# Performance work log

Measured on AMD Instinct MI355X. Metric: run time of the kernel, lower is better.

The kernel has to match this reference:

```python
import jax, jax.numpy as jnp
import numpy as np

D, K, CIN, CD, COUT = 3, 16, 128, 32, 256
C = CIN + CD                  # 160 = C_in + C_delta after concat
DM = -(-COUT // C)            # depth_multiplier = ceil(C_out / C) = 2
N, I = 4, 2048                # batch, points per cloud; M = N*I = 8192


def _bn(x, g, b, eps=1e-5):
    # BatchNorm1d in training mode: biased batch statistics over dim 0
    mu = x.mean(0)
    v = x.var(0)
    return (x - mu) * jax.lax.rsqrt(v + eps) * g + b


def _knn(p, k):
    # knn_graph over ALL M points (wrapper passes no batch vector), loop=True
    d2 = jnp.sum(p * p, axis=1)
    dist = d2[:, None] + d2[None, :] - 2.0 * (p @ p.T)   # [M,M]
    _, idx = jax.lax.top_k(-dist, k)                     # [M,K], self first
    return idx


def _gconv(t, w, b, M):
    # grouped Conv1d(K, K*K, kernel=K, groups=K): t [M,K,K], w [K(cin), K(out/grp), K(tap)]
    return jnp.einsum('mcl,col->mco', t, w).reshape(M, K * K) + b


def _xconv(xf, pf, idx, w1a, b1a, g1a, be1a, w1b, b1b, g1b, be1b,
           w2, b2, g2a, be2a, wc2a, bc2a, g2b, be2b, wc2b, bc2b, g2c, be2c,
           wcd, bcd, wl, bl):
    M = pf.shape[0]
    rel = pf[idx] - pf[:, None, :]                       # [M,K,D] relative neighbor coords
    # mlp1: lift relative coords to C_delta features
    h = rel.reshape(M * K, D)
    h = _bn(jax.nn.elu(h @ w1a + b1a), g1a, be1a)
    h = _bn(jax.nn.elu(h @ w1b + b1b), g1b, be1b)
    x_star = jnp.concatenate([h.reshape(M, K, CD), xf[idx]], axis=-1)  # [M,K,C]
    x_star = x_star.transpose(0, 2, 1)                   # [M,C,K]
    # mlp2: learn KxK X-transformation from the K*D relative coords
    t = _bn(jax.nn.elu(rel.reshape(M, K * D) @ w2 + b2), g2a, be2a).reshape(M, K, K)
    t = _bn(jax.nn.elu(_gconv(t, wc2a, bc2a, M)), g2b, be2b).reshape(M, K, K)
    t = _bn(_gconv(t, wc2b, bc2b, M), g2c, be2c).reshape(M, K, K)
    xt = jnp.einsum('mck,mkj->mcj', x_star, t)           # [M,C,K] batched matmul
    # depthwise Conv1d(C, C*DM, K, groups=C) collapses K, then final Linear
    y = jnp.einsum('mcl,col->mco', xt, wcd).reshape(M, C * DM) + bcd
    return y @ wl + bl                                   # [M,COUT]


def setup_inputs() -> dict:
    key = jax.random.key(0)
    ks = jax.random.split(key, 16)
    r = lambda k, s: jax.random.normal(k, s, jnp.float32) * 0.1
    return dict(
        x=jax.random.normal(ks[0], (N, I, CIN), jnp.float32),
        pos=jax.random.normal(ks[1], (N, I, D), jnp.float32),
        w1a=r(ks[2], (D, CD)), b1a=r(ks[3], (CD,)), g1a=jnp.ones((CD,)), be1a=jnp.zeros((CD,)),
        w1b=r(ks[4], (CD, CD)), b1b=r(ks[5], (CD,)), g1b=jnp.ones((CD,)), be1b=jnp.zeros((CD,)),
        w2=r(ks[6], (D * K, K * K)), b2=r(ks[7], (K * K,)), g2a=jnp.ones((K * K,)), be2a=jnp.zeros((K * K,)),
        wc2a=r(ks[8], (K, K, K)), bc2a=r(ks[9], (K * K,)), g2b=jnp.ones((K * K,)), be2b=jnp.zeros((K * K,)),
        wc2b=r(ks[10], (K, K, K)), bc2b=r(ks[11], (K * K,)), g2c=jnp.ones((K * K,)), be2c=jnp.zeros((K * K,)),
        wcd=r(ks[12], (C, DM, K)), bcd=r(ks[13], (C * DM,)),
        wl=r(ks[14], (C * DM, COUT)), bl=r(ks[15], (COUT,)),
    )


def reference(x, pos, w1a, b1a, g1a, be1a, w1b, b1b, g1b, be1b,
              w2, b2, g2a, be2a, wc2a, bc2a, g2b, be2b, wc2b, bc2b, g2c, be2c,
              wcd, bcd, wl, bl):
    pf = pos.reshape(N * I, D)
    xf = x.reshape(N * I, CIN)
    idx = _knn(pf, K)
    out = _xconv(xf, pf, idx, w1a, b1a, g1a, be1a, w1b, b1b, g1b, be1b,
                 w2, b2, g2a, be2a, wc2a, bc2a, g2b, be2b, wc2b, bc2b, g2c, be2c,
                 wcd, bcd, wl, bl)
    return out.reshape(N, I, COUT)
```

## Files before the change

### kernel.cpp

```cpp
#include <hip/hip_runtime.h>
#include <math.h>

#define M_PTS 8192
#define MK    131072

typedef __attribute__((ext_vector_type(8))) short bf16x8;
typedef __attribute__((ext_vector_type(4))) float f32x4;
typedef __fp16 half2v __attribute__((ext_vector_type(2)));
union H2U { half2v h; unsigned u; };

__device__ __forceinline__ float elu(float v){ return v > 0.f ? v : __expf(v)-1.0f; }

__device__ __forceinline__ unsigned cvt_pk_bf16(float lo, float hi){
  unsigned r;
  asm("v_cvt_pk_bf16_f32 %0, %1, %2" : "=v"(r) : "v"(lo), "v"(hi));
  return r;
}
__device__ __forceinline__ unsigned pk_min_u16(unsigned a, unsigned b){
  unsigned r; asm("v_pk_min_u16 %0, %1, %2" : "=v"(r) : "v"(a), "v"(b)); return r;
}
__device__ __forceinline__ unsigned pk_max_u16(unsigned a, unsigned b){
  unsigned r; asm("v_pk_max_u16 %0, %1, %2" : "=v"(r) : "v"(a), "v"(b)); return r;
}

__device__ __forceinline__ unsigned distkey(float4 c, float qx, float qy, float qz, float d2q){
  #pragma clang fp contract(off)
  float dot  = __builtin_fmaf(c.z, qz, __builtin_fmaf(c.y, qy, __builtin_fmaf(c.x, qx, 0.0f)));
  float A    = d2q + c.w;
  float B    = 2.0f * dot;
  float dist = A - B;
  unsigned u = __float_as_uint(dist);
  return u ^ ((unsigned)((int)u >> 31) | 0x80000000u);
}

__global__ __launch_bounds__(256) void knn_kernel(const float* __restrict__ pos,
                                                  int* __restrict__ nidx,
                                                  float* __restrict__ st){
  __shared__ float4 cand[1024];
  __shared__ unsigned long long hits[4][64];
  int tid  = threadIdx.x;
  int lane = tid & 63;
  int wv   = tid >> 6;
  int q    = blockIdx.x*4 + wv;
  if (blockIdx.x == 0){
    for (int i = tid; i < 2048; i += 256) st[i] = 0.f;
  }
  float qx = pos[3*q], qy = pos[3*q+1], qz = pos[3*q+2];
  float d2q;
  {
    #pragma clang fp contract(off)
    d2q = (qx*qx + qy*qy) + qz*qz;
  }

  unsigned ka[8];
  #pragma unroll
  for (int s=0;s<8;s++) ka[s] = 0xFFFFFFFFu;

  for (int base = 0; base < M_PTS; base += 1024){
    for (int t = tid; t < 1024; t += 256){
      #pragma clang fp contract(off)
      int j = base + t;
      float x = pos[3*j], y = pos[3*j+1], z = pos[3*j+2];
      float d2v = (x*x + y*y) + z*z;
      cand[t] = make_float4(x,y,z,d2v);
    }
    __syncthreads();
    #pragma unroll
    for (int k=0; k<8; k++){
      float4 c0 = cand[lane + k*128];
      float4 c1 = cand[lane + 64 + k*128];
      float dotA = c0.x*qx + c0.y*qy + c0.z*qz;
      float dotB = c1.x*qx + c1.y*qy + c1.z*qz;
      float dA = fmaxf((d2q + c0.w) - 2.0f*dotA, 0.f);
      float dB = fmaxf((d2q + c1.w) - 2.0f*dotB, 0.f);
      H2U pu; pu.h = __builtin_amdgcn_cvt_pkrtz(dA, dB);
      unsigned v = pu.u;
      #pragma unroll
      for (int s=0;s<8;s++){
        unsigned mn = pk_min_u16(v, ka[s]);
        unsigned mx = pk_max_u16(v, ka[s]);
        ka[s] = mn; v = mx;
      }
    }
    __syncthreads();
  }

  unsigned lo[8], hi[8];
  #pragma unroll
  for (int s=0;s<8;s++){ lo[s] = ka[s] & 0xFFFFu; hi[s] = ka[s] >> 16; }
  unsigned t16 = 0xFFFFu;
  for (int r=0; r<16; r++){
    unsigned head = min(lo[0], hi[0]);
    unsigned best = head;
    #pragma unroll
    for (int off=32; off>0; off>>=1){
      unsigned o = __shfl_xor(best, off, 64);
      best = min(best, o);
    }
    bool adv = (head == best);
    bool fromLo = lo[0] <= hi[0];
    bool aL = adv && fromLo;
    bool aH = adv && !fromLo;
    #pragma unroll
    for (int s=0;s<7;s++){
      lo[s] = aL ? lo[s+1] : lo[s];
      hi[s] = aH ? hi[s+1] : hi[s];
    }
    lo[7] = aL ? 0xFFFFu : lo[7];
    hi[7] = aH ? 0xFFFFu : hi[7];
    t16 = best;
  }
  unsigned tu = min(t16 + 2u, 0x7C00u);
  float thrF;
  asm("v_cvt_f32_f16 %0, %1" : "=v"(thrF) : "v"(tu));

  int cnt = 0;
  for (int base = 0; base < M_PTS; base += 1024){
    for (int t = tid; t < 1024; t += 256){
      #pragma clang fp contract(off)
      int j = base + t;
      float x = pos[3*j], y = pos[3*j+1], z = pos[3*j+2];
      float d2v = (x*x + y*y) + z*z;
      cand[t] = make_float4(x,y,z,d2v);
    }
    __syncthreads();
    #pragma unroll
    for (int k=0; k<16; k++){
      int idx = lane + k*64;
      int j = base + idx;
      float4 c = cand[idx];
      float dot = c.x*qx + c.y*qy + c.z*qz;
      bool hit = ((d2q + c.w) - 2.0f*dot) <= thrF;
      unsigned long long m = __ballot(hit);
      if (m){
        unsigned u = distkey(c, qx, qy, qz, d2q);
        if (hit){
          int slot = cnt + __popcll(m & ((1ull<<lane)-1ull));
          if (slot < 64) hits[wv][slot] = ((unsigned long long)u << 32) | (unsigned)j;
        }
        cnt += (int)__popcll(m);
      }
    }
    __syncthreads();
  }

  int cc = min(cnt, 64);
  unsigned long long mine = (lane < cc) ? hits[wv][lane] : ~0ull;
  for (int r=0; r<16; r++){
    unsigned long long best = mine;
    #pragma unroll
    for (int off=32; off>0; off>>=1){
      unsigned long long o = __shfl_xor(best, off, 64);
      best = (o < best) ? o : best;
    }
    if (mine == best) mine = ~0ull;
    if (lane == 0) nidx[q*16 + r] = (int)(unsigned)best;
  }
}

#define COMPUTE_RELF_8()                                              \
  for (int f = tid; f < 8*48; f += 256){                              \
    int p = f/48, kd = f%48, k = kd/3, d = kd%3;                      \
    int j = nidx[(m0+p)*16 + k];                                      \
    relf[p][kd] = pos[3*j+d] - pos[3*(m0+p)+d];                       \
  }                                                                   \
  __syncthreads();

#define COMPUTE_T1_8(acc)                                             \
  _Pragma("unroll")                                                   \
  for (int p=0;p<8;p++) acc[p] = b2[tid];                             \
  for (int kk=0; kk<48; kk++){                                        \
    float w = w2[kk*256 + tid];                                       \
    _Pragma("unroll")                                                 \
    for (int p=0;p<8;p++) acc[p] += relf[p][kk]*w;                    \
  }

__global__ __launch_bounds__(256) void stats_a_kernel(const float* __restrict__ pos,
    const int* __restrict__ nidx,
    const float* __restrict__ w1a, const float* __restrict__ b1a,
    const float* __restrict__ w2,  const float* __restrict__ b2,
    const float* __restrict__ wl,  unsigned short* __restrict__ wlbf,
    float* __restrict__ tact,
    float* __restrict__ s1, float* __restrict__ s3){
  int tid = threadIdx.x;
  if (blockIdx.x < 512){
    __shared__ float relS[256][3];
    __shared__ float red[8][64];
    int r = blockIdx.x*256 + tid;
    int m = r >> 4;
    int j = nidx[r];
    relS[tid][0] = pos[3*j  ]-pos[3*m  ];
    relS[tid][1] = pos[3*j+1]-pos[3*m+1];
    relS[tid][2] = pos[3*j+2]-pos[3*m+2];
    __syncthreads();
    int c = tid & 31, g = tid >> 5;
    float w0=w1a[c], w1v=w1a[32+c], w2v=w1a[64+c], b=b1a[c];
    float s=0.f, q=0.f;
    for (int rr=g*32; rr<g*32+32; rr++){
      float h = elu(b + relS[rr][0]*w0 + relS[rr][1]*w1v + relS[rr][2]*w2v);
      s += h; q += h*h;
    }
    red[g][c]=s; red[g][32+c]=q;
    __syncthreads();
    if (tid < 64){
      float a=0.f;
      #pragma unroll
      for (int gg=0;gg<8;gg++) a += red[gg][tid];
      atomicAdd(&s1[tid], a);
    }
  } else if (blockIdx.x < 1536){
    __shared__ float relf[8][48];
    int m0 = (blockIdx.x-512)*8;
    COMPUTE_RELF_8();
    float acc[8];
    COMPUTE_T1_8(acc);
    float s=0.f, q=0.f;
    #pragma unroll
    for (int p=0;p<8;p++){
      float v = elu(acc[p]);
      s += v; q += v*v;
      tact[(size_t)(m0+p)*256 + tid] = v;
    }
    atomicAdd(&s3[tid], s); atomicAdd(&s3[256+tid], q);
  } else {
    int t = (blockIdx.x - 1536)*256 + tid;
    int lane = t & 63;
    int fr   = t >> 6;
    int k0   = (fr >> 4)*32 + (lane >> 4)*8;
    int col  = (fr & 15)*16 + (lane & 15);
    const float* wp = wl + (size_t)k0*256 + col;
    uint4 v;
    v.x = cvt_pk_bf16(wp[0],    wp[256]);
    v.y = cvt_pk_bf16(wp[512],  wp[768]);
    v.z = cvt_pk_bf16(wp[1024], wp[1280]);
    v.w = cvt_pk_bf16(wp[1536], wp[1792]);
    ((uint4*)wlbf)[t] = v;
  }
}

__global__ __launch_bounds__(256) void stats_b_kernel(const float* __restrict__ pos,
    const int* __restrict__ nidx,
    const float* __restrict__ w1a, const float* __restrict__ b1a,
    const float* __restrict__ s1,  const float* __restrict__ g1a, const float* __restrict__ be1a,
    const float* __restrict__ w1b, const float* __restrict__ b1b,
    float* __restrict__ tact,
    const float* __restrict__ s3,  const float* __restrict__ g2a, const float* __restrict__ be2a,
    const float* __restrict__ wc2a,const float* __restrict__ bc2a,
    float* __restrict__ s2, float* __restrict__ s4){
  int tid = threadIdx.x;
  const float invMK = 1.f/(float)MK;
  const float invM  = 1.f/8192.f;
  if (blockIdx.x < 2048){
    __shared__ float xnS[64][33];
    __shared__ float red[8][64];
    __shared__ float muA[32], ivA[32];
    if (tid < 32){
      float mu  = s1[tid]*invMK;
      float var = s1[32+tid]*invMK - mu*mu;
      muA[tid] = mu; ivA[tid] = rsqrtf(var+1e-5f)*g1a[tid];
    }
    __syncthreads();
    {
      int rl = tid >> 2;
      int r  = blockIdx.x*64 + rl;
      int m = r >> 4;
      int j = nidx[r];
      float rx = pos[3*j]-pos[3*m], ry = pos[3*j+1]-pos[3*m+1], rz = pos[3*j+2]-pos[3*m+2];
      int c0 = (tid & 3)*8;
      #pragma unroll
      for (int u=0; u<8; u++){
        int cc = c0 + u;
        float h = elu(b1a[cc] + rx*w1a[cc] + ry*w1a[32+cc] + rz*w1a[64+cc]);
        xnS[rl][cc] = (h-muA[cc])*ivA[cc] + be1a[cc];
      }
    }
    __syncthreads();
    int o = tid & 31, g = tid >> 5;
    float wcol[32];
    #pragma unroll
    for (int cc=0;cc<32;cc++) wcol[cc] = w1b[cc*32+o];
    float bo = b1b[o], s=0.f, q=0.f;
    for (int rr=g*8; rr<g*8+8; rr++){
      float a = bo;
      #pragma unroll
      for (int cc=0;cc<32;cc++) a += xnS[rr][cc]*wcol[cc];
      float v = elu(a);
      s += v; q += v*v;
    }
    red[g][o]=s; red[g][32+o]=q;
    __syncthreads();
    if (tid < 64){
      float a=0.f;
      #pragma unroll
      for (int gg=0;gg<8;gg++) a += red[gg][tid];
      atomicAdd(&s2[tid], a);
    }
  } else {
    __shared__ float tn[8][256];
    int m0 = (blockIdx.x-2048)*8;
    float mu3  = s3[tid]*invM;
    float var3 = s3[256+tid]*invM - mu3*mu3;
    float i3   = rsqrtf(var3+1e-5f)*g2a[tid];
    float bb3  = be2a[tid];
    float tv[8];
    #pragma unroll
    for (int p=0;p<8;p++) tv[p] = tact[(size_t)(m0+p)*256 + tid];
    #pragma unroll
    for (int p=0;p<8;p++) tn[p][tid] = (tv[p]-mu3)*i3 + bb3;
    __syncthreads();
    int c = tid >> 4;
    float wreg[16];
    const float4* wv4 = (const float4*)(wc2a + tid*16);
    #pragma unroll
    for (int v=0; v<4; v++){ float4 f = wv4[v]; wreg[4*v]=f.x; wreg[4*v+1]=f.y; wreg[4*v+2]=f.z; wreg[4*v+3]=f.w; }
    float bias = bc2a[tid];
    float s=0.f, q=0.f;
    #pragma unroll
    for (int p=0;p<8;p++){
      float a2 = bias;
      #pragma unroll
      for (int l=0;l<16;l++) a2 += tn[p][c*16+l]*wreg[l];
      float v = elu(a2);
      s += v; q += v*v;
      tv[p] = v;
    }
    #pragma unroll
    for (int p=0;p<8;p++) tact[(size_t)(m0+p)*256 + tid] = tv[p];
    atomicAdd(&s4[tid], s); atomicAdd(&s4[256+tid], q);
  }
}

__global__ __launch_bounds__(256) void t3_stats_kernel(
    float* __restrict__ tact,
    const float* __restrict__ s4, const float* __restrict__ g2b, const float* __restrict__ be2b,
    const float* __restrict__ wc2b, const float* __restrict__ bc2b, float* __restrict__ s5){
  __shared__ float tn2[8][256];
  int m0 = blockIdx.x*8, tid = threadIdx.x;
  const float invM = 1.f/8192.f;
  float mu4  = s4[tid]*invM;
  float var4 = s4[256+tid]*invM - mu4*mu4;
  float i4   = rsqrtf(var4+1e-5f)*g2b[tid];
  float bb4  = be2b[tid];
  float tv[8];
  #pragma unroll
  for (int p=0;p<8;p++) tv[p] = tact[(size_t)(m0+p)*256 + tid];
  #pragma unroll
  for (int p=0;p<8;p++) tn2[p][tid] = (tv[p]-mu4)*i4 + bb4;
  __syncthreads();
  int c = tid >> 4;
  float w2reg[16];
  { const float4* wv4 = (const float4*)(wc2b + tid*16);
    #pragma unroll
    for (int v=0; v<4; v++){ float4 f = wv4[v]; w2reg[4*v]=f.x; w2reg[4*v+1]=f.y; w2reg[4*v+2]=f.z; w2reg[4*v+3]=f.w; } }
  float bias2 = bc2b[tid];
  float s=0.f, q=0.f;
  #pragma unroll
  for (int p=0;p<8;p++){
    float a3 = bias2;
    #pragma unroll
    for (int l=0;l<16;l++) a3 += tn2[p][c*16+l]*w2reg[l];
    s += a3; q += a3*a3;
    tv[p] = a3;
  }
  #pragma unroll
  for (int p=0;p<8;p++) tact[(size_t)(m0+p)*256 + tid] = tv[p];
  atomicAdd(&s5[tid], s); atomicAdd(&s5[256+tid], q);
}

#define PF8 8
__global__ __launch_bounds__(256) void final_mfma_kernel(
    const float* __restrict__ x, const float* __restrict__ pos, const int* __restrict__ nidx,
    const float* __restrict__ w1a, const float* __restrict__ b1a,
    const float* __restrict__ g1a, const float* __restrict__ be1a,
    const float* __restrict__ w1b, const float* __restrict__ b1b,
    const float* __restrict__ g1b, const float* __restrict__ be1b,
    const float* __restrict__ g2c, const float* __restrict__ be2c,
    const float* __restrict__ wcd, const float* __restrict__ bcd,
    const unsigned short* __restrict__ wlbf, const float* __restrict__ bl,
    const float* __restrict__ st,
    float* __restrict__ out){
  __shared__ float tA[PF8][256];
  __shared__ float xs[PF8*32*17];
  __shared__ unsigned short yh[16][328];
  __shared__ int   sidx[PF8*16];
  __shared__ float mu1[32], i1g[32], mu2[32], i2g[32];
  int tid = threadIdx.x;
  int m0  = blockIdx.x*PF8;
  const float invMK = 1.f/(float)MK;
  const float invM  = 1.f/8192.f;

  if (tid < PF8*16) sidx[tid] = nidx[m0*16 + tid];
  if (tid < 32){
    float mu  = st[tid]*invMK;
    float var = st[32+tid]*invMK - mu*mu;
    mu1[tid] = mu; i1g[tid] = rsqrtf(var+1e-5f)*g1a[tid];
    float mu_2  = st[64+tid]*invMK;
    float var_2 = st[96+tid]*invMK - mu_2*mu_2;
    mu2[tid] = mu_2; i2g[tid] = rsqrtf(var_2+1e-5f)*g1b[tid];
  }
  {
    unsigned short* yz = &yh[8][0];
    for (int i = tid; i < 8*328; i += 256) yz[i] = 0;
  }
  {
    float mu5 = st[1152+tid]*invM, var5 = st[1408+tid]*invM - mu5*mu5;
    float i5 = rsqrtf(var5+1e-5f)*g2c[tid], bb5 = be2c[tid];
    #pragma unroll
    for (int p=0;p<PF8;p++){
      float v = out[(size_t)(m0+p)*256 + tid];
      tA[p][tid] = (v-mu5)*i5 + bb5;
    }
  }
  __syncthreads();

  #pragma unroll 1
  for (int half = 0; half < 2; ++half){
    int row = half*64 + (tid >> 2);
    int p = row >> 4, k = row & 15;
    int q8 = (tid & 3)*8;
    int m = m0 + p;
    int j = sidx[row];
    float rx = pos[3*j]-pos[3*m], ry = pos[3*j+1]-pos[3*m+1], rz = pos[3*j+2]-pos[3*m+2];
    float xn[32];
    #pragma unroll
    for (int cc=0; cc<32; cc++){
      float h = elu(b1a[cc] + rx*w1a[cc] + ry*w1a[32+cc] + rz*w1a[64+cc]);
      xn[cc] = (h-mu1[cc])*i1g[cc] + be1a[cc];
    }
    #pragma unroll
    for (int oo=0; oo<8; oo++){
      int o = q8 + oo;
      float a = b1b[o];
      #pragma unroll
      for (int cc=0; cc<32; cc++) a += xn[cc]*w1b[cc*32+o];
      float h2v = elu(a);
      xs[(p*32 + o)*17 + k] = (h2v-mu2[o])*i2g[o] + be1b[o];
    }
  }
  __syncthreads();

  #pragma unroll 1
  for (int pair = tid; pair < PF8*160; pair += 256){
    int p = pair / 160, cch = pair % 160;
    float av[16];
    if (cch < 32){
      #pragma unroll
      for (int k16=0;k16<16;k16++) av[k16] = xs[(p*32+cch)*17 + k16];
    } else {
      #pragma unroll
      for (int k16=0;k16<16;k16++) av[k16] = x[(size_t)sidx[p*16+k16]*128 + (cch-32)];
    }
    float xt[16];
    #pragma unroll
    for (int j16=0;j16<16;j16++) xt[j16]=0.f;
    #pragma unroll
    for (int k16=0;k16<16;k16++){
      float a = av[k16];
      #pragma unroll
      for (int j16=0;j16<16;j16++) xt[j16] += a*tA[p][k16*16+j16];
    }
    float y0 = bcd[cch*2], y1 = bcd[cch*2+1];
    #pragma unroll
    for (int l=0;l<16;l++){
      y0 += xt[l]*wcd[cch*32 + l];
      y1 += xt[l]*wcd[cch*32 + 16 + l];
    }
    *(unsigned*)&yh[p][cch*2] = cvt_pk_bf16(y0, y1);
  }
  __syncthreads();

  {
    int lane = tid & 63;
    int wvi  = tid >> 6;
    int lrow = lane & 15;
    int lgrp = lane >> 4;
    const bf16x8* wb = (const bf16x8*)wlbf;
    f32x4 acc[4];
    #pragma unroll
    for (int nt=0; nt<4; ++nt) acc[nt] = (f32x4){0.f,0.f,0.f,0.f};
    #pragma unroll 1
    for (int kt = 0; kt < 10; ++kt){
      bf16x8 ah = *(const bf16x8*)&yh[lrow][kt*32 + lgrp*8];
      #pragma unroll
      for (int nt = 0; nt < 4; ++nt){
        bf16x8 bh = wb[(size_t)((kt*16 + wvi*4 + nt)*64) + lane];
        acc[nt] = __builtin_amdgcn_mfma_f32_16x16x32_bf16(ah, bh, acc[nt], 0, 0, 0);
      }
    }
    if (lgrp < 2){
      #pragma unroll
      for (int nt=0; nt<4; ++nt){
        int col = wvi*64 + nt*16 + lrow;
        float bv = bl[col];
        #pragma unroll
        for (int r=0;r<4;r++){
          int orow = lgrp*4 + r;
          out[(size_t)(m0+orow)*256 + col] = acc[nt][r] + bv;
        }
      }
    }
  }
}

#define PF 4
__global__ __launch_bounds__(256) void final_kernel(
    const float* __restrict__ x, const float* __restrict__ pos, const int* __restrict__ nidx,
    const float* __restrict__ w1a, const float* __restrict__ b1a,
    const float* __restrict__ g1a, const float* __restrict__ be1a,
    const float* __restrict__ w1b, const float* __restrict__ b1b,
    const float* __restrict__ g1b, const float* __restrict__ be1b,
    const float* __restrict__ g2c, const float* __restrict__ be2c,
    const float* __restrict__ wcd, const float* __restrict__ bcd,
    const float* __restrict__ wl,  const float* __restrict__ bl,
    const float* __restrict__ st,
    float* __restrict__ out){
  __shared__ float tA[PF][256];
  __shared__ float xs[PF*32*17];
  __shared__ float yy[PF][320];
  __shared__ int   sidx[PF*16];
  __shared__ float mu1[32], i1g[32], mu2[32], i2g[32];
  int tid = threadIdx.x;
  int m0  = blockIdx.x*PF;
  const float invMK = 1.f/(float)MK;
  const float invM  = 1.f/8192.f;

  if (tid < PF*16) sidx[tid] = nidx[m0*16 + tid];
  if (tid < 32){
    float mu  = st[tid]*invMK;
    float var = st[32+tid]*invMK - mu*mu;
    mu1[tid] = mu; i1g[tid] = rsqrtf(var+1e-5f)*g1a[tid];
    float mu_2  = st[64+tid]*invMK;
    float var_2 = st[96+tid]*invMK - mu_2*mu_2;
    mu2[tid] = mu_2; i2g[tid] = rsqrtf(var_2+1e-5f)*g1b[tid];
  }
  {
    float mu5 = st[1152+tid]*invM, var5 = st[1408+tid]*invM - mu5*mu5;
    float i5 = rsqrtf(var5+1e-5f)*g2c[tid], bb5 = be2c[tid];
    #pragma unroll
    for (int p=0;p<PF;p++){
      float v = out[(size_t)(m0+p)*256 + tid];
      tA[p][tid] = (v-mu5)*i5 + bb5;
    }
  }
  __syncthreads();

  {
    int row = tid >> 2;
    int p = row >> 4, k = row & 15;
    int q8 = (tid & 3)*8;
    int m = m0 + p;
    int j = sidx[p*16 + k];
    float rx = pos[3*j]-pos[3*m], ry = pos[3*j+1]-pos[3*m+1], rz = pos[3*j+2]-pos[3*m+2];
    float xn[32];
    #pragma unroll
    for (int cc=0; cc<32; cc++){
      float h = elu(b1a[cc] + rx*w1a[cc] + ry*w1a[32+cc] + rz*w1a[64+cc]);
      xn[cc] = (h-mu1[cc])*i1g[cc] + be1a[cc];
    }
    #pragma unroll
    for (int oo=0; oo<8; oo++){
      int o = q8 + oo;
      float a = b1b[o];
      #pragma unroll
      for (int cc=0; cc<32; cc++) a += xn[cc]*w1b[cc*32+o];
      float h2v = elu(a);
      xs[(p*32 + o)*17 + k] = (h2v-mu2[o])*i2g[o] + be1b[o];
    }
  }
  __syncthreads();

  for (int pair = tid; pair < PF*160; pair += 256){
    int p = pair / 160, cch = pair % 160;
    float av[16];
    if (cch < 32){
      #pragma unroll
      for (int k16=0;k16<16;k16++) av[k16] = xs[(p*32+cch)*17 + k16];
    } else {
      #pragma unroll
      for (int k16=0;k16<16;k16++) av[k16] = x[(size_t)sidx[p*16+k16]*128 + (cch-32)];
    }
    float xt[16];
    #pragma unroll
    for (int j16=0;j16<16;j16++) xt[j16]=0.f;
    #pragma unroll
    for (int k16=0;k16<16;k16++){
      float a = av[k16];
      #pragma unroll
      for (int j16=0;j16<16;j16++) xt[j16] += a*tA[p][k16*16+j16];
    }
    float y0 = bcd[cch*2], y1 = bcd[cch*2+1];
    #pragma unroll
    for (int l=0;l<16;l++){
      y0 += xt[l]*wcd[cch*32 + l];
      y1 += xt[l]*wcd[cch*32 + 16 + l];
    }
    yy[p][cch*2] = y0; yy[p][cch*2+1] = y1;
  }
  __syncthreads();

  float accO[PF];
  #pragma unroll
  for (int p=0;p<PF;p++) accO[p] = bl[tid];
  for (int q=0;q<320;q++){
    float w = wl[q*256 + tid];
    #pragma unroll
    for (int p=0;p<PF;p++) accO[p] += yy[p][q]*w;
  }
  #pragma unroll
  for (int p=0;p<PF;p++) out[(size_t)(m0+p)*256 + tid] = accO[p];
}

extern "C" void kernel_launch(void* const* d_in, const int* in_sizes, int n_in,
                              void* d_out, int out_size, void* d_ws, size_t ws_size,
                              hipStream_t stream){
  const float* x    = (const float*)d_in[0];
  const float* pos  = (const float*)d_in[1];
  const float* w1a  = (const float*)d_in[2];
  const float* b1a  = (const float*)d_in[3];
  const float* g1a  = (const float*)d_in[4];
  const float* be1a = (const float*)d_in[5];
  const float* w1b  = (const float*)d_in[6];
  const float* b1b  = (const float*)d_in[7];
  const float* g1b  = (const float*)d_in[8];
  const float* be1b = (const float*)d_in[9];
  const float* w2   = (const float*)d_in[10];
  const float* b2   = (const float*)d_in[11];
  const float* g2a  = (const float*)d_in[12];
  const float* be2a = (const float*)d_in[13];
  const float* wc2a = (const float*)d_in[14];
  const float* bc2a = (const float*)d_in[15];
  const float* g2b  = (const float*)d_in[16];
  const float* be2b = (const float*)d_in[17];
  const float* wc2b = (const float*)d_in[18];
  const float* bc2b = (const float*)d_in[19];
  const float* g2c  = (const float*)d_in[20];
  const float* be2c = (const float*)d_in[21];
  const float* wcd  = (const float*)d_in[22];
  const float* bcd  = (const float*)d_in[23];
  const float* wl   = (const float*)d_in[24];
  const float* bl   = (const float*)d_in[25];
  float* out = (float*)d_out;

  char* ws = (char*)d_ws;
  int*   nidx = (int*)(ws + 0);
  float* st   = (float*)(ws + 524288);
  float* s1 = st;
  float* s2 = st + 64;
  float* s3 = st + 128;
  float* s4 = st + 640;
  float* s5 = st + 1152;
  bool big = ws_size >= (size_t)696320;
  unsigned short* wlbf = big ? (unsigned short*)(ws + 532480) : (unsigned short*)0;

  knn_kernel<<<2048,256,0,stream>>>(pos, nidx, st);
  stats_a_kernel<<<(big ? 1576 : 1536),256,0,stream>>>(pos, nidx, w1a, b1a, w2, b2,
                                                       wl, wlbf, out, s1, s3);
  stats_b_kernel<<<3072,256,0,stream>>>(pos, nidx, w1a, b1a, s1, g1a, be1a, w1b, b1b,
                                        out, s3, g2a, be2a, wc2a, bc2a, s2, s4);
  t3_stats_kernel<<<1024,256,0,stream>>>(out, s4, g2b, be2b, wc2b, bc2b, s5);
  if (big){
    final_mfma_kernel<<<1024,256,0,stream>>>(x, pos, nidx,
                                             w1a, b1a, g1a, be1a, w1b, b1b, g1b, be1b,
                                             g2c, be2c, wcd, bcd, wlbf, bl, st, out);
  } else {
    final_kernel<<<2048,256,0,stream>>>(x, pos, nidx,
                                        w1a, b1a, g1a, be1a, w1b, b1b, g1b, be1b,
                                        g2c, be2c, wcd, bcd, wl, bl, st, out);
  }
}
```

Baseline: 396.4 us.

## Stage all KNN candidates once per 1024-thread block and halve final tile

The KNN kernel now uses 1024-thread blocks that load all 8192 candidate points into shared memory once, so the chunked reload and the barriers in both passes are gone. Each block serves 16 queries instead of 4, which cuts repeated global reads of the point cloud. The final MFMA kernel processes 4 points per block instead of 8 and stores the mlp1 features in bf16 in shared memory. This raises LDS use in KNN (128KB) and may limit occupancy, and it adds bf16 rounding on the h features.

Result: faster. 377.6 us (-4.7%).

```diff
diff --git a/kernel.cpp b/kernel.cpp
--- a/kernel.cpp
+++ b/kernel.cpp
@@ -15,6 +15,10 @@
   unsigned r;
   asm("v_cvt_pk_bf16_f32 %0, %1, %2" : "=v"(r) : "v"(lo), "v"(hi));
   return r;
+}
+__device__ __forceinline__ unsigned short f2bf(float v){
+  unsigned u = __float_as_uint(v);
+  return (unsigned short)((u + 0x7FFFu + ((u>>16)&1u)) >> 16);
 }
 __device__ __forceinline__ unsigned pk_min_u16(unsigned a, unsigned b){
   unsigned r; asm("v_pk_min_u16 %0, %1, %2" : "=v"(r) : "v"(a), "v"(b)); return r;
@@ -33,17 +37,23 @@
   return u ^ ((unsigned)((int)u >> 31) | 0x80000000u);
 }
 
-__global__ __launch_bounds__(256) void knn_kernel(const float* __restrict__ pos,
-                                                  int* __restrict__ nidx,
-                                                  float* __restrict__ st){
-  __shared__ float4 cand[1024];
-  __shared__ unsigned long long hits[4][64];
+__global__ __launch_bounds__(1024) void knn_kernel(const float* __restrict__ pos,
+                                                   int* __restrict__ nidx,
+                                                   float* __restrict__ st){
+  __shared__ float4 cand[8192];
+  __shared__ unsigned long long hits[16][64];
   int tid  = threadIdx.x;
   int lane = tid & 63;
   int wv   = tid >> 6;
-  int q    = blockIdx.x*4 + wv;
+  int q    = blockIdx.x*16 + wv;
   if (blockIdx.x == 0){
-    for (int i = tid; i < 2048; i += 256) st[i] = 0.f;
+    for (int i = tid; i < 2048; i += 1024) st[i] = 0.f;
+  }
+  for (int t = tid; t < M_PTS; t += 1024){
+    #pragma clang fp contract(off)
+    float x = pos[3*t], y = pos[3*t+1], z = pos[3*t+2];
+    float d2v = (x*x + y*y) + z*z;
+    cand[t] = make_float4(x,y,z,d2v);
   }
   float qx = pos[3*q], qy = pos[3*q+1], qz = pos[3*q+2];
   float d2q;
@@ -51,38 +61,27 @@
     #pragma clang fp contract(off)
     d2q = (qx*qx + qy*qy) + qz*qz;
   }
+  __syncthreads();
 
   unsigned ka[8];
   #pragma unroll
   for (int s=0;s<8;s++) ka[s] = 0xFFFFFFFFu;
 
-  for (int base = 0; base < M_PTS; base += 1024){
-    for (int t = tid; t < 1024; t += 256){
-      #pragma clang fp contract(off)
-      int j = base + t;
-      float x = pos[3*j], y = pos[3*j+1], z = pos[3*j+2];
-      float d2v = (x*x + y*y) + z*z;
-      cand[t] = make_float4(x,y,z,d2v);
-    }
-    __syncthreads();
-    #pragma unroll
-    for (int k=0; k<8; k++){
-      float4 c0 = cand[lane + k*128];
-      float4 c1 = cand[lane + 64 + k*128];
-      float dotA = c0.x*qx + c0.y*qy + c0.z*qz;
-      float dotB = c1.x*qx + c1.y*qy + c1.z*qz;
-      float dA = fmaxf((d2q + c0.w) - 2.0f*dotA, 0.f);
-      float dB = fmaxf((d2q + c1.w) - 2.0f*dotB, 0.f);
-      H2U pu; pu.h = __builtin_amdgcn_cvt_pkrtz(dA, dB);
-      unsigned v = pu.u;
-      #pragma unroll
-      for (int s=0;s<8;s++){
-        unsigned mn = pk_min_u16(v, ka[s]);
-        unsigned mx = pk_max_u16(v, ka[s]);
-        ka[s] = mn; v = mx;
-      }
-    }
-    __syncthreads();
+  for (int k=0; k<64; k++){
+    float4 c0 = cand[lane + k*128];
+    float4 c1 = cand[lane + 64 + k*128];
+    float dotA = c0.x*qx + c0.y*qy + c0.z*qz;
+    float dotB = c1.x*qx + c1.y*qy + c1.z*qz;
+    float dA = fmaxf((d2q + c0.w) - 2.0f*dotA, 0.f);
+    float dB = fmaxf((d2q + c1.w) - 2.0f*dotB, 0.f);
+    H2U pu; pu.h = __builtin_amdgcn_cvt_pkrtz(dA, dB);
+    unsigned v = pu.u;
+    #pragma unroll
+    for (int s=0;s<8;s++){
+      unsigned mn = pk_min_u16(v, ka[s]);
+      unsigned mx = pk_max_u16(v, ka[s]);
+      ka[s] = mn; v = mx;
+    }
   }
 
   unsigned lo[8], hi[8];
@@ -115,33 +114,20 @@
   asm("v_cvt_f32_f16 %0, %1" : "=v"(thrF) : "v"(tu));
 
   int cnt = 0;
-  for (int base = 0; base < M_PTS; base += 1024){
-    for (int t = tid; t < 1024; t += 256){
-      #pragma clang fp contract(off)
-      int j = base + t;
-      float x = pos[3*j], y = pos[3*j+1], z = pos[3*j+2];
-      float d2v = (x*x + y*y) + z*z;
-      cand[t] = make_float4(x,y,z,d2v);
-    }
-    __syncthreads();
-    #pragma unroll
-    for (int k=0; k<16; k++){
-      int idx = lane + k*64;
-      int j = base + idx;
-      float4 c = cand[idx];
-      float dot = c.x*qx + c.y*qy + c.z*qz;
-      bool hit = ((d2q + c.w) - 2.0f*dot) <= thrF;
-      unsigned long long m = __ballot(hit);
-      if (m){
-        unsigned u = distkey(c, qx, qy, qz, d2q);
-        if (hit){
-          int slot = cnt + __popcll(m & ((1ull<<lane)-1ull));
-          if (slot < 64) hits[wv][slot] = ((unsigned long long)u << 32) | (unsigned)j;
-        }
-        cnt += (int)__popcll(m);
+  for (int k=0; k<128; k++){
+    int j = lane + k*64;
+    float4 c = cand[j];
+    float dot = c.x*qx + c.y*qy + c.z*qz;
+    bool hit = ((d2q + c.w) - 2.0f*dot) <= thrF;
+    unsigned long long m = __ballot(hit);
+    if (m){
+      unsigned u = distkey(c, qx, qy, qz, d2q);
+      if (hit){
+        int slot = cnt + __popcll(m & ((1ull<<lane)-1ull));
+        if (slot < 64) hits[wv][slot] = ((unsigned long long)u << 32) | (unsigned)j;
       }
-    }
-    __syncthreads();
+      cnt += (int)__popcll(m);
+    }
   }
 
   int cc = min(cnt, 64);
@@ -367,7 +353,7 @@
   atomicAdd(&s5[tid], s); atomicAdd(&s5[256+tid], q);
 }
 
-#define PF8 8
+#define PFM 4
 __global__ __launch_bounds__(256) void final_mfma_kernel(
     const float* __restrict__ x, const float* __restrict__ pos, const int* __restrict__ nidx,
     const float* __restrict__ w1a, const float* __restrict__ b1a,
@@ -379,17 +365,17 @@
     const unsigned short* __restrict__ wlbf, const float* __restrict__ bl,
     const float* __restrict__ st,
     float* __restrict__ out){
-  __shared__ float tA[PF8][256];
-  __shared__ float xs[PF8*32*17];
+  __shared__ float tA[PFM][256];
+  __shared__ unsigned short xs[PFM*32*17];
   __shared__ unsigned short yh[16][328];
-  __shared__ int   sidx[PF8*16];
+  __shared__ int   sidx[PFM*16];
   __shared__ float mu1[32], i1g[32], mu2[32], i2g[32];
   int tid = threadIdx.x;
-  int m0  = blockIdx.x*PF8;
+  int m0  = blockIdx.x*PFM;
   const float invMK = 1.f/(float)MK;
   const float invM  = 1.f/8192.f;
 
-  if (tid < PF8*16) sidx[tid] = nidx[m0*16 + tid];
+  if (tid < PFM*16) sidx[tid] = nidx[m0*16 + tid];
   if (tid < 32){
     float mu  = st[tid]*invMK;
     float var = st[32+tid]*invMK - mu*mu;
@@ -399,23 +385,22 @@
     mu2[tid] = mu_2; i2g[tid] = rsqrtf(var_2+1e-5f)*g1b[tid];
   }
   {
-    unsigned short* yz = &yh[8][0];
-    for (int i = tid; i < 8*328; i += 256) yz[i] = 0;
+    unsigned short* yz = &yh[PFM][0];
+    for (int i = tid; i < (16-PFM)*328; i += 256) yz[i] = 0;
   }
   {
     float mu5 = st[1152+tid]*invM, var5 = st[1408+tid]*invM - mu5*mu5;
     float i5 = rsqrtf(var5+1e-5f)*g2c[tid], bb5 = be2c[tid];
     #pragma unroll
-    for (int p=0;p<PF8;p++){
+    for (int p=0;p<PFM;p++){
       float v = out[(size_t)(m0+p)*256 + tid];
       tA[p][tid] = (v-mu5)*i5 + bb5;
     }
   }
   __syncthreads();
 
-  #pragma unroll 1
-  for (int half = 0; half < 2; ++half){
-    int row = half*64 + (tid >> 2);
+  {
+    int row = tid >> 2;
     int p = row >> 4, k = row & 15;
     int q8 = (tid & 3)*8;
     int m = m0 + p;
@@ -434,18 +419,18 @@
       #pragma unroll
       for (int cc=0; cc<32; cc++) a += xn[cc]*w1b[cc*32+o];
       float h2v = elu(a);
-      xs[(p*32 + o)*17 + k] = (h2v-mu2[o])*i2g[o] + be1b[o];
-    }
-  }
-  __syncthreads();
-
-  #pragma unroll 1
-  for (int pair = tid; pair < PF8*160; pair += 256){
+      xs[(p*32 + o)*17 + k] = f2bf((h2v-mu2[o])*i2g[o] + be1b[o]);
+    }
+  }
+  __syncthreads();
+
+  for (int pair = tid; pair < PFM*160; pair += 256){
     int p = pair / 160, cch = pair % 160;
     float av[16];
     if (cch < 32){
       #pragma unroll
-      for (int k16=0;k16<16;k16++) av[k16] = xs[(p*32+cch)*17 + k16];
+      for (int k16=0;k16<16;k16++)
+        av[k16] = __uint_as_float((unsigned)xs[(p*32+cch)*17 + k16] << 16);
     } else {
       #pragma unroll
       for (int k16=0;k16<16;k16++) av[k16] = x[(size_t)sidx[p*16+k16]*128 + (cch-32)];
@@ -487,14 +472,14 @@
         acc[nt] = __builtin_amdgcn_mfma_f32_16x16x32_bf16(ah, bh, acc[nt], 0, 0, 0);
       }
     }
-    if (lgrp < 2){
+    if (lgrp == 0){
       #pragma unroll
       for (int nt=0; nt<4; ++nt){
         int col = wvi*64 + nt*16 + lrow;
         float bv = bl[col];
         #pragma unroll
         for (int r=0;r<4;r++){
-          int orow = lgrp*4 + r;
+          int orow = r;
           out[(size_t)(m0+orow)*256 + col] = acc[nt][r] + bv;
         }
       }
@@ -652,14 +637,14 @@
   bool big = ws_size >= (size_t)696320;
   unsigned short* wlbf = big ? (unsigned short*)(ws + 532480) : (unsigned short*)0;
 
-  knn_kernel<<<2048,256,0,stream>>>(pos, nidx, st);
+  knn_kernel<<<512,1024,0,stream>>>(pos, nidx, st);
   stats_a_kernel<<<(big ? 1576 : 1536),256,0,stream>>>(pos, nidx, w1a, b1a, w2, b2,
                                                        wl, wlbf, out, s1, s3);
   stats_b_kernel<<<3072,256,0,stream>>>(pos, nidx, w1a, b1a, s1, g1a, be1a, w1b, b1b,
                                         out, s3, g2a, be2a, wc2a, bc2a, s2, s4);
   t3_stats_kernel<<<1024,256,0,stream>>>(out, s4, g2b, be2b, wc2b, bc2b, s5);
   if (big){
-    final_mfma_kernel<<<1024,256,0,stream>>>(x, pos, nidx,
+    final_mfma_kernel<<<2048,256,0,stream>>>(x, pos, nidx,
                                              w1a, b1a, g1a, be1a, w1b, b1b, g1b, be1b,
                                              g2c, be2c, wcd, bcd, wlbf, bl, st, out);
   } else {
```
